# Kernel tuning notes

Hardware: AMD Instinct MI355X
Metric: run time of the kernel (lower is better)

## Reference

```python
import jax, jax.numpy as jnp
import numpy as np

EPS = 1e-6


def setup_inputs() -> dict:
    key = jax.random.key(0)
    k1, = jax.random.split(key, 1)
    N = 8192
    X = jax.random.normal(k1, (1, N, 3), dtype=jnp.float32) * 10.0  # Ca coords, Angstrom-ish scale
    mask = jnp.ones((1, N), dtype=jnp.float32)
    return {"X": X, "mask": mask, "top_k": 30}


def reference(X, mask, top_k):
    # mask_2D: [B, N, N]
    mask_2D = mask[:, None, :] * mask[:, :, None]
    # pairwise distances: [B, N, N]
    dX = X[:, None, :, :] - X[:, :, None, :]            # [B, N, N, 3]
    D = mask_2D * jnp.sqrt(jnp.sum(dX * dX, axis=-1) + EPS)
    D_max = jnp.max(D, axis=-1, keepdims=True)
    D_adjust = D + 2.0 * (1.0 - mask_2D) * D_max        # push masked pairs far away
    k = min(top_k, X.shape[-2])
    # smallest-k via top_k on negated distances
    neg_D, E_idx = jax.lax.top_k(-D_adjust, k)          # [B, N, k]
    D_neighbors = -neg_D
    # gather_edges on mask_2D[..., None]: [B, N, k, 1]
    mask_neighbors = jnp.take_along_axis(mask_2D[..., None], E_idx[..., None], axis=2)
    return (D_neighbors, E_idx, mask_neighbors)
```

## Files before the change

### kernel.cpp

```cpp
#include <hip/hip_runtime.h>
#include <math.h>
#include <stdint.h>

#define NPTS 8192
#define TOPK 30
#define BUFSZ 1024
#define SENT 0xFFFFFFFFFFFFFFFFULL

__device__ __forceinline__ unsigned long long exact_key(const float* __restrict__ X,
                                                        float xi, float yi, float zi, int j) {
#pragma clang fp contract(off)
    float dx = X[j * 3 + 0] - xi;
    float dy = X[j * 3 + 1] - yi;
    float dz = X[j * 3 + 2] - zi;
    float d2 = dx * dx;
    d2 = d2 + dy * dy;
    d2 = d2 + dz * dz;
    float d = sqrtf(d2 + 1e-6f);
    return ((unsigned long long)__float_as_uint(d) << 32) | (unsigned int)j;
}

__device__ __forceinline__ unsigned long long bcast64(unsigned long long v, int src) {
    return (unsigned long long)__shfl((long long)v, src);
}

__global__ __launch_bounds__(256)
void knn_topk_kernel(const float* __restrict__ X,
                     const float* __restrict__ mask,
                     float* __restrict__ out)
{
    __shared__ int buf[4][BUFSZ];

    const int lane = threadIdx.x & 63;
    const int wv   = threadIdx.x >> 6;
    const int row  = (int)(blockIdx.x << 2) | wv;

    const float xi = X[row * 3 + 0];
    const float yi = X[row * 3 + 1];
    const float zi = X[row * 3 + 2];

    float smin = INFINITY;
#pragma unroll
    for (int k = 0; k < 4; ++k) {
        const int j = (lane + 64 * k) * 32;
        const float dx = X[j * 3 + 0] - xi;
        const float dy = X[j * 3 + 1] - yi;
        const float dz = X[j * 3 + 2] - zi;
        const float q = fmaf(dz, dz, fmaf(dy, dy, dx * dx));
        smin = fminf(smin, q);
    }
#pragma unroll
    for (int k = 2; k <= 64; k <<= 1) {
#pragma unroll
        for (int m = k >> 1; m >= 1; m >>= 1) {
            const float p = __shfl_xor(smin, m);
            const bool take_min = (((lane & k) == 0) == ((lane & m) == 0));
            smin = ((smin < p) == take_min) ? smin : p;
        }
    }
    float T = __shfl(smin, 3);

    const float4* X4 = (const float4*)X;
    int C;
    for (;;) {
        C = 0;
        for (int t = 0; t < NPTS / 256; ++t) {
            const int cbase = t * 256 + (lane << 2);
            const int bi = (t * 64 + lane) * 3;
            const float4 a0 = X4[bi + 0];
            const float4 a1 = X4[bi + 1];
            const float4 a2 = X4[bi + 2];

            const float dx0 = a0.x - xi, dy0 = a0.y - yi, dz0 = a0.z - zi;
            const float dx1 = a0.w - xi, dy1 = a1.x - yi, dz1 = a1.y - zi;
            const float dx2 = a1.z - xi, dy2 = a1.w - yi, dz2 = a2.x - zi;
            const float dx3 = a2.y - xi, dy3 = a2.z - yi, dz3 = a2.w - zi;

            const float q0 = fmaf(dz0, dz0, fmaf(dy0, dy0, dx0 * dx0));
            const float q1 = fmaf(dz1, dz1, fmaf(dy1, dy1, dx1 * dx1));
            const float q2 = fmaf(dz2, dz2, fmaf(dy2, dy2, dx2 * dx2));
            const float q3 = fmaf(dz3, dz3, fmaf(dy3, dy3, dx3 * dx3));

            const bool p0 = q0 < T;
            const bool p1 = q1 < T;
            const bool p2 = q2 < T;
            const bool p3 = q3 < T;

#pragma unroll
            for (int k = 0; k < 4; ++k) {
                const bool pk = (k == 0) ? p0 : (k == 1) ? p1 : (k == 2) ? p2 : p3;
                const unsigned long long ball = __ballot(pk);
                const int myoff = C + __popcll(ball & ((1ull << lane) - 1ull));
                if (pk && myoff < BUFSZ) buf[wv][myoff] = cbase + k;
                C += __popcll(ball);
            }
        }
        if (C >= 33 && C <= BUFSZ) break;
        T = (C < 33) ? T * 2.0f : T * 0.5f;
    }

    unsigned long long list = SENT;
    for (int s0 = 0; s0 < C; s0 += 64) {
        const int s = s0 + lane;
        unsigned long long ck = SENT;
        if (s < C) ck = exact_key(X, xi, yi, zi, buf[wv][s]);

#pragma unroll
        for (int k = 2; k <= 64; k <<= 1) {
#pragma unroll
            for (int m = k >> 1; m >= 1; m >>= 1) {
                const unsigned long long p = (unsigned long long)__shfl_xor((long long)ck, m);
                const bool take_min = (((lane & k) == 0) == ((lane & m) == 0));
                ck = ((ck < p) == take_min) ? ck : p;
            }
        }

        const unsigned long long cg = bcast64(ck, 63 - lane);
        unsigned long long v = (lane < TOPK) ? list : cg;
#pragma unroll
        for (int m = 32; m >= 1; m >>= 1) {
            const unsigned long long p = (unsigned long long)__shfl_xor((long long)v, m);
            const bool low = ((lane & m) == 0);
            const bool lt = (v < p);
            v = (low == lt) ? v : p;
        }
        list = (lane < TOPK) ? v : SENT;
    }

    if (lane < TOPK) {
        const int   li = (int)(uint32_t)(list & 0xFFFFFFFFu);
        const float lv = __uint_as_float((uint32_t)(list >> 32));
        const int base = row * TOPK + lane;
        out[base]                   = lv;
        out[NPTS * TOPK + base]     = (float)li;
        out[2 * NPTS * TOPK + base] = mask[row] * mask[li];
    }
}

extern "C" void kernel_launch(void* const* d_in, const int* in_sizes, int n_in,
                              void* d_out, int out_size, void* d_ws, size_t ws_size,
                              hipStream_t stream) {
    const float* X    = (const float*)d_in[0];
    const float* mask = (const float*)d_in[1];
    float* out        = (float*)d_out;

    dim3 grid(NPTS / 4), block(256);
    knn_topk_kernel<<<grid, block, 0, stream>>>(X, mask, out);
}
```

Before: 110.5 us.

## Process two query rows per wavefront with dual thresholds and bitmask candidate compaction

Each wavefront now handles two query rows, so every loaded X tile is reused for both rows and the grid is halved. The threshold is estimated from a larger 512-point sample, and two candidate thresholds (tight and loose) are tested in a single pass, which cuts down on re-scan iterations. Candidate flags are packed into per-lane bitmasks and compacted after counting with a prefix scan, replacing a ballot per element. A correctness check on the 30th distance against the threshold triggers a retry. The trade-offs are more register pressure and divergence between the two rows, plus a smaller per-row buffer.

```diff
diff --git a/kernel.cpp b/kernel.cpp
--- a/kernel.cpp
+++ b/kernel.cpp
@@ -4,7 +4,7 @@
 
 #define NPTS 8192
 #define TOPK 30
-#define BUFSZ 1024
+#define BUFSZ 768
 #define SENT 0xFFFFFFFFFFFFFFFFULL
 
 __device__ __forceinline__ unsigned long long exact_key(const float* __restrict__ X,
@@ -29,111 +29,188 @@
                      const float* __restrict__ mask,
                      float* __restrict__ out)
 {
-    __shared__ int buf[4][BUFSZ];
+    __shared__ int buf2[4][2][BUFSZ];
 
     const int lane = threadIdx.x & 63;
     const int wv   = threadIdx.x >> 6;
-    const int row  = (int)(blockIdx.x << 2) | wv;
-
-    const float xi = X[row * 3 + 0];
-    const float yi = X[row * 3 + 1];
-    const float zi = X[row * 3 + 2];
-
-    float smin = INFINITY;
-#pragma unroll
-    for (int k = 0; k < 4; ++k) {
-        const int j = (lane + 64 * k) * 32;
-        const float dx = X[j * 3 + 0] - xi;
-        const float dy = X[j * 3 + 1] - yi;
-        const float dz = X[j * 3 + 2] - zi;
-        const float q = fmaf(dz, dz, fmaf(dy, dy, dx * dx));
-        smin = fminf(smin, q);
+    const int gw   = (int)(blockIdx.x << 2) | wv;
+    const int row0 = gw * 2, row1 = row0 + 1;
+
+    const float xi0 = X[row0*3+0], yi0 = X[row0*3+1], zi0 = X[row0*3+2];
+    const float xi1 = X[row1*3+0], yi1 = X[row1*3+1], zi1 = X[row1*3+2];
+
+    float s0 = INFINITY, s1 = INFINITY;
+#pragma unroll
+    for (int k = 0; k < 8; ++k) {
+        const int j = lane + (k << 6);
+        const float px = X[j*3+0], py = X[j*3+1], pz = X[j*3+2];
+        float dx = px - xi0, dy = py - yi0, dz = pz - zi0;
+        s0 = fminf(s0, fmaf(dz, dz, fmaf(dy, dy, dx * dx)));
+        dx = px - xi1; dy = py - yi1; dz = pz - zi1;
+        s1 = fminf(s1, fmaf(dz, dz, fmaf(dy, dy, dx * dx)));
     }
 #pragma unroll
     for (int k = 2; k <= 64; k <<= 1) {
 #pragma unroll
         for (int m = k >> 1; m >= 1; m >>= 1) {
-            const float p = __shfl_xor(smin, m);
-            const bool take_min = (((lane & k) == 0) == ((lane & m) == 0));
-            smin = ((smin < p) == take_min) ? smin : p;
-        }
-    }
-    float T = __shfl(smin, 3);
+            const float p0 = __shfl_xor(s0, m);
+            const float p1 = __shfl_xor(s1, m);
+            const bool tm = (((lane & k) == 0) == ((lane & m) == 0));
+            s0 = ((s0 < p0) == tm) ? s0 : p0;
+            s1 = ((s1 < p1) == tm) ? s1 : p1;
+        }
+    }
+    float Tt0 = __shfl(s0, 6), Tl0 = __shfl(s0, 19);
+    float Tt1 = __shfl(s1, 6), Tl1 = __shfl(s1, 19);
 
     const float4* X4 = (const float4*)X;
-    int C;
+    unsigned long long list0 = SENT, list1 = SENT;
+    bool need0 = true, need1 = true;
+
     for (;;) {
-        C = 0;
-        for (int t = 0; t < NPTS / 256; ++t) {
-            const int cbase = t * 256 + (lane << 2);
-            const int bi = (t * 64 + lane) * 3;
-            const float4 a0 = X4[bi + 0];
-            const float4 a1 = X4[bi + 1];
-            const float4 a2 = X4[bi + 2];
-
-            const float dx0 = a0.x - xi, dy0 = a0.y - yi, dz0 = a0.z - zi;
-            const float dx1 = a0.w - xi, dy1 = a1.x - yi, dz1 = a1.y - zi;
-            const float dx2 = a1.z - xi, dy2 = a1.w - yi, dz2 = a2.x - zi;
-            const float dx3 = a2.y - xi, dy3 = a2.z - yi, dz3 = a2.w - zi;
-
-            const float q0 = fmaf(dz0, dz0, fmaf(dy0, dy0, dx0 * dx0));
-            const float q1 = fmaf(dz1, dz1, fmaf(dy1, dy1, dx1 * dx1));
-            const float q2 = fmaf(dz2, dz2, fmaf(dy2, dy2, dx2 * dx2));
-            const float q3 = fmaf(dz3, dz3, fmaf(dy3, dy3, dx3 * dx3));
-
-            const bool p0 = q0 < T;
-            const bool p1 = q1 < T;
-            const bool p2 = q2 < T;
-            const bool p3 = q3 < T;
-
-#pragma unroll
-            for (int k = 0; k < 4; ++k) {
-                const bool pk = (k == 0) ? p0 : (k == 1) ? p1 : (k == 2) ? p2 : p3;
-                const unsigned long long ball = __ballot(pk);
-                const int myoff = C + __popcll(ball & ((1ull << lane) - 1ull));
-                if (pk && myoff < BUFSZ) buf[wv][myoff] = cbase + k;
-                C += __popcll(ball);
+        unsigned mt0[4], ml0[4], mt1[4], ml1[4];
+        int ct0 = 0, cl0 = 0, ct1 = 0, cl1 = 0;
+#pragma unroll
+        for (int w = 0; w < 4; ++w) {
+            unsigned wt0 = 0, wl0 = 0, wt1 = 0, wl1 = 0;
+#pragma unroll 2
+            for (int t8 = 0; t8 < 8; ++t8) {
+                const int t = (w << 3) + t8;
+                const int bi = (t * 64 + lane) * 3;
+                const float4 a0 = X4[bi + 0];
+                const float4 a1 = X4[bi + 1];
+                const float4 a2 = X4[bi + 2];
+                if (need0) {
+                    const float dx0 = a0.x-xi0, dy0 = a0.y-yi0, dz0 = a0.z-zi0;
+                    const float dx1 = a0.w-xi0, dy1 = a1.x-yi0, dz1 = a1.y-zi0;
+                    const float dx2 = a1.z-xi0, dy2 = a1.w-yi0, dz2 = a2.x-zi0;
+                    const float dx3 = a2.y-xi0, dy3 = a2.z-yi0, dz3 = a2.w-zi0;
+                    const float q0 = fmaf(dz0,dz0,fmaf(dy0,dy0,dx0*dx0));
+                    const float q1 = fmaf(dz1,dz1,fmaf(dy1,dy1,dx1*dx1));
+                    const float q2 = fmaf(dz2,dz2,fmaf(dy2,dy2,dx2*dx2));
+                    const float q3 = fmaf(dz3,dz3,fmaf(dy3,dy3,dx3*dx3));
+                    unsigned nt = (q0<Tt0)?1u:0u; nt |= (q1<Tt0)?2u:0u;
+                    nt |= (q2<Tt0)?4u:0u;        nt |= (q3<Tt0)?8u:0u;
+                    unsigned nl = (q0<Tl0)?1u:0u; nl |= (q1<Tl0)?2u:0u;
+                    nl |= (q2<Tl0)?4u:0u;        nl |= (q3<Tl0)?8u:0u;
+                    wt0 |= nt << (t8*4);  wl0 |= nl << (t8*4);
+                }
+                if (need1) {
+                    const float dx0 = a0.x-xi1, dy0 = a0.y-yi1, dz0 = a0.z-zi1;
+                    const float dx1 = a0.w-xi1, dy1 = a1.x-yi1, dz1 = a1.y-zi1;
+                    const float dx2 = a1.z-xi1, dy2 = a1.w-yi1, dz2 = a2.x-zi1;
+                    const float dx3 = a2.y-xi1, dy3 = a2.z-yi1, dz3 = a2.w-zi1;
+                    const float q0 = fmaf(dz0,dz0,fmaf(dy0,dy0,dx0*dx0));
+                    const float q1 = fmaf(dz1,dz1,fmaf(dy1,dy1,dx1*dx1));
+                    const float q2 = fmaf(dz2,dz2,fmaf(dy2,dy2,dx2*dx2));
+                    const float q3 = fmaf(dz3,dz3,fmaf(dy3,dy3,dx3*dx3));
+                    unsigned nt = (q0<Tt1)?1u:0u; nt |= (q1<Tt1)?2u:0u;
+                    nt |= (q2<Tt1)?4u:0u;        nt |= (q3<Tt1)?8u:0u;
+                    unsigned nl = (q0<Tl1)?1u:0u; nl |= (q1<Tl1)?2u:0u;
+                    nl |= (q2<Tl1)?4u:0u;        nl |= (q3<Tl1)?8u:0u;
+                    wt1 |= nt << (t8*4);  wl1 |= nl << (t8*4);
+                }
             }
-        }
-        if (C >= 33 && C <= BUFSZ) break;
-        T = (C < 33) ? T * 2.0f : T * 0.5f;
-    }
-
-    unsigned long long list = SENT;
-    for (int s0 = 0; s0 < C; s0 += 64) {
-        const int s = s0 + lane;
-        unsigned long long ck = SENT;
-        if (s < C) ck = exact_key(X, xi, yi, zi, buf[wv][s]);
-
-#pragma unroll
-        for (int k = 2; k <= 64; k <<= 1) {
-#pragma unroll
-            for (int m = k >> 1; m >= 1; m >>= 1) {
-                const unsigned long long p = (unsigned long long)__shfl_xor((long long)ck, m);
-                const bool take_min = (((lane & k) == 0) == ((lane & m) == 0));
-                ck = ((ck < p) == take_min) ? ck : p;
-            }
-        }
-
-        const unsigned long long cg = bcast64(ck, 63 - lane);
-        unsigned long long v = (lane < TOPK) ? list : cg;
-#pragma unroll
-        for (int m = 32; m >= 1; m >>= 1) {
-            const unsigned long long p = (unsigned long long)__shfl_xor((long long)v, m);
-            const bool low = ((lane & m) == 0);
-            const bool lt = (v < p);
-            v = (low == lt) ? v : p;
-        }
-        list = (lane < TOPK) ? v : SENT;
+            mt0[w]=wt0; ml0[w]=wl0; mt1[w]=wt1; ml1[w]=wl1;
+            ct0 += __popc(wt0); cl0 += __popc(wl0);
+            ct1 += __popc(wt1); cl1 += __popc(wl1);
+        }
+#pragma unroll
+        for (int d = 32; d; d >>= 1) {
+            ct0 += __shfl_xor(ct0, d); cl0 += __shfl_xor(cl0, d);
+            ct1 += __shfl_xor(ct1, d); cl1 += __shfl_xor(cl1, d);
+        }
+
+#define RESOLVE(R)                                                             \
+    if (need##R) {                                                             \
+        const bool tOK = (ct##R >= 33) && (ct##R <= BUFSZ);                    \
+        const bool lOK = (cl##R >= 33) && (cl##R <= BUFSZ);                    \
+        if (tOK || lOK) {                                                      \
+            const int   C  = tOK ? ct##R : cl##R;                              \
+            const float Tu = tOK ? Tt##R : Tl##R;                              \
+            int mycnt = 0;                                                     \
+            _Pragma("unroll")                                                  \
+            for (int w = 0; w < 4; ++w)                                        \
+                mycnt += __popc(tOK ? mt##R[w] : ml##R[w]);                    \
+            int s = mycnt;                                                     \
+            _Pragma("unroll")                                                  \
+            for (int d = 1; d < 64; d <<= 1) {                                 \
+                const int n = __shfl_up(s, d);                                 \
+                if (lane >= d) s += n;                                         \
+            }                                                                  \
+            int off = s - mycnt;                                               \
+            _Pragma("unroll")                                                  \
+            for (int w = 0; w < 4; ++w) {                                      \
+                unsigned mm = tOK ? mt##R[w] : ml##R[w];                       \
+                while (mm) {                                                   \
+                    const int b = __builtin_ctz(mm);                           \
+                    mm &= mm - 1;                                              \
+                    buf2[wv][R][off++] =                                       \
+                        ((w << 3) + (b >> 2)) * 256 + (lane << 2) + (b & 3);   \
+                }                                                              \
+            }                                                                  \
+            unsigned long long lst = SENT;                                     \
+            for (int c0 = 0; c0 < C; c0 += 64) {                               \
+                const int sc = c0 + lane;                                      \
+                unsigned long long ck = SENT;                                  \
+                if (sc < C) ck = exact_key(X, xi##R, yi##R, zi##R,             \
+                                           buf2[wv][R][sc]);                   \
+                _Pragma("unroll")                                              \
+                for (int k = 2; k <= 64; k <<= 1) {                            \
+                    _Pragma("unroll")                                          \
+                    for (int m = k >> 1; m >= 1; m >>= 1) {                    \
+                        const unsigned long long p =                           \
+                            (unsigned long long)__shfl_xor((long long)ck, m);  \
+                        const bool tm =                                        \
+                            (((lane & k) == 0) == ((lane & m) == 0));          \
+                        ck = ((ck < p) == tm) ? ck : p;                        \
+                    }                                                          \
+                }                                                              \
+                const unsigned long long cg = bcast64(ck, 63 - lane);          \
+                unsigned long long v = (lane < TOPK) ? lst : cg;               \
+                _Pragma("unroll")                                              \
+                for (int m = 32; m >= 1; m >>= 1) {                            \
+                    const unsigned long long p =                               \
+                        (unsigned long long)__shfl_xor((long long)v, m);       \
+                    const bool low = ((lane & m) == 0);                        \
+                    v = (low == (v < p)) ? v : p;                              \
+                }                                                              \
+                lst = (lane < TOPK) ? v : SENT;                                \
+            }                                                                  \
+            const float D30 = __uint_as_float(                                 \
+                (uint32_t)(bcast64(lst, TOPK - 1) >> 32));                     \
+            if (fmaf(D30, D30, -1e-6f) < Tu * 0.99995f) {                      \
+                list##R = lst; need##R = false;                                \
+            } else { Tt##R *= 2.0f; Tl##R *= 2.0f; }                           \
+        } else {                                                               \
+            Tt##R = (ct##R < 33) ? Tt##R * 2.0f : Tt##R * 0.5f;                \
+            Tl##R = (cl##R < 33) ? Tl##R * 2.0f : Tl##R * 0.5f;                \
+        }                                                                      \
+    }
+
+        RESOLVE(0)
+        RESOLVE(1)
+#undef RESOLVE
+        if (!need0 && !need1) break;
     }
 
     if (lane < TOPK) {
-        const int   li = (int)(uint32_t)(list & 0xFFFFFFFFu);
-        const float lv = __uint_as_float((uint32_t)(list >> 32));
-        const int base = row * TOPK + lane;
-        out[base]                   = lv;
-        out[NPTS * TOPK + base]     = (float)li;
-        out[2 * NPTS * TOPK + base] = mask[row] * mask[li];
+        {
+            const int   li = (int)(uint32_t)(list0 & 0xFFFFFFFFu);
+            const float lv = __uint_as_float((uint32_t)(list0 >> 32));
+            const int base = row0 * TOPK + lane;
+            out[base]                   = lv;
+            out[NPTS * TOPK + base]     = (float)li;
+            out[2 * NPTS * TOPK + base] = mask[row0] * mask[li];
+        }
+        {
+            const int   li = (int)(uint32_t)(list1 & 0xFFFFFFFFu);
+            const float lv = __uint_as_float((uint32_t)(list1 >> 32));
+            const int base = row1 * TOPK + lane;
+            out[base]                   = lv;
+            out[NPTS * TOPK + base]     = (float)li;
+            out[2 * NPTS * TOPK + base] = mask[row1] * mask[li];
+        }
     }
 }
 
@@ -144,6 +221,6 @@
     const float* mask = (const float*)d_in[1];
     float* out        = (float*)d_out;
 
-    dim3 grid(NPTS / 4), block(256);
+    dim3 grid(NPTS / 8), block(256);
     knn_topk_kernel<<<grid, block, 0, stream>>>(X, mask, out);
 }
```

Result: no change. 111.3 us (+0.7%).
